# Optimization experiments

Hardware: AMD Instinct MI355X
Metric: run time of the kernel (lower is better)

The kernel has to match this reference:

```python
import jax, jax.numpy as jnp
import numpy as np

B, T, D, W, H = 64, 512, 768, 255, 8
DH = D // H

def layernorm(x, g, b, eps=1e-5):
    m = jnp.mean(x, axis=-1, keepdims=True)
    v = jnp.mean((x - m) ** 2, axis=-1, keepdims=True)
    return (x - m) * jax.lax.rsqrt(v + eps) * g + b

def setup_inputs() -> dict:
    key = jax.random.key(0)
    ks = list(jax.random.split(key, 12))
    p = lambda k, shape, s=0.02: (jax.random.normal(k, shape, jnp.float32) * s)
    # words_ids: -100 at CLS/SEP, each word spans 2 subtokens -> 255 words/row
    wi = np.full((B, T), -100, dtype=np.int32)
    pos = np.arange(1, T - 1)
    wi[:, 1:T - 1] = (pos - 1) // 2
    return {
        'output_bert': jax.random.normal(ks[0], (B, T, D), jnp.float32),
        'words_ids': jnp.asarray(wi),
        'Wq': p(ks[1], (D, D)), 'bq': jnp.zeros((D,), jnp.float32),
        'Wk': p(ks[2], (D, D)), 'bk': jnp.zeros((D,), jnp.float32),
        'Wv': p(ks[3], (D, D)), 'bv': jnp.zeros((D,), jnp.float32),
        'Wo': p(ks[4], (D, D)), 'bo': jnp.zeros((D,), jnp.float32),
        'ln1_g': jnp.ones((D,), jnp.float32), 'ln1_b': jnp.zeros((D,), jnp.float32),
        'W1f': p(ks[5], (D, 4 * D)), 'b1f': jnp.zeros((4 * D,), jnp.float32),
        'W2f': p(ks[6], (4 * D, D)), 'b2f': jnp.zeros((D,), jnp.float32),
        'ln2_g': jnp.ones((D,), jnp.float32), 'ln2_b': jnp.zeros((D,), jnp.float32),
        'ng': jnp.ones((D,), jnp.float32), 'nb': jnp.zeros((D,), jnp.float32),
        'lin_w': p(ks[7], (D, 2)), 'lin_b': jnp.zeros((2,), jnp.float32),
    }

def reference(output_bert, words_ids, Wq, bq, Wk, bk, Wv, bv, Wo, bo,
              ln1_g, ln1_b, W1f, b1f, W2f, b2f, ln2_g, ln2_b, ng, nb, lin_w, lin_b):
    Bsz = output_bert.shape[0]
    # --- first-subtoken gather: first token position of each word id ---
    hits = words_ids[:, None, :] == jnp.arange(W)[None, :, None]   # [B, W, T]
    first_idx = jnp.argmax(hits, axis=-1)                           # [B, W]
    feat = jnp.take_along_axis(output_bert, first_idx[..., None], axis=1)  # [B, W, D]
    # --- transformer encoder layer (post-norm, relu FFN) ---
    q = (feat @ Wq + bq).reshape(Bsz, W, H, DH)
    k = (feat @ Wk + bk).reshape(Bsz, W, H, DH)
    v = (feat @ Wv + bv).reshape(Bsz, W, H, DH)
    scores = jnp.einsum('bqhd,bkhd->bhqk', q, k) * (1.0 / np.sqrt(DH))
    attn = jax.nn.softmax(scores, axis=-1)
    ctx = jnp.einsum('bhqk,bkhd->bqhd', attn, v).reshape(Bsz, W, D)
    x = layernorm(feat + ctx @ Wo + bo, ln1_g, ln1_b)
    ff = jax.nn.relu(x @ W1f + b1f) @ W2f + b2f
    x = layernorm(x + ff, ln2_g, ln2_b)
    # --- final LayerNorm + Linear + softmax + argmax path ---
    x = layernorm(x, ng, nb)
    logits = x @ lin_w + lin_b
    ner_prob = jax.nn.softmax(logits, axis=-1)
    path = jnp.argmax(ner_prob, axis=-1)
    return ner_prob, path
```

## Files before the change

### kernel.cpp

```cpp
#include <hip/hip_runtime.h>
#include <cmath>

#define Bsz 64
#define Tt  512
#define Dd  768
#define Wn  255
#define Hh  8
#define DHd 96
#define NROWS (Bsz*Wn)

typedef _Float16 half_t;
typedef _Float16 f16x8 __attribute__((ext_vector_type(8)));
typedef _Float16 f16x4 __attribute__((ext_vector_type(4)));
typedef float f32x4 __attribute__((ext_vector_type(4)));

#define OFF_QKV 0
#define OFF_WO  5308416
#define OFF_W1  7077888
#define OFF_W2  14155776
#define W2_CSTR 3538944
#define SLOTH 25165824
__device__ __align__(16) half_t g_w16[21233664];

__device__ __forceinline__ void gload16(const half_t* g, half_t* l) {
    __builtin_amdgcn_global_load_lds((const __attribute__((address_space(1))) void*)g,
                                     (__attribute__((address_space(3))) void*)l, 16, 0, 0);
}

template<int N> __device__ __forceinline__ void waitv() {
    if constexpr (N == 0) asm volatile("s_waitcnt vmcnt(0)" ::: "memory");
    else if constexpr (N == 1) asm volatile("s_waitcnt vmcnt(1)" ::: "memory");
    else if constexpr (N == 2) asm volatile("s_waitcnt vmcnt(2)" ::: "memory");
    else if constexpr (N == 4) asm volatile("s_waitcnt vmcnt(4)" ::: "memory");
}


__global__ void k_init_fi(int* fi) {
    int i = blockIdx.x * 256 + threadIdx.x;
    if (i < Bsz * Wn) fi[i] = 0x7fffffff;
}

__global__ void k_scan(const int* __restrict__ wid, int* __restrict__ fi) {
    int i = blockIdx.x * 256 + threadIdx.x;
    if (i >= Bsz * Tt) return;
    int b = i / Tt, t = i % Tt;
    int w = wid[i];
    if (w >= 0 && w < Wn) atomicMin(&fi[b * Wn + w], t);
}

__global__ void k_bcat(const float* __restrict__ bq, const float* __restrict__ bk,
                       const float* __restrict__ bv, float* __restrict__ o) {
    int i = blockIdx.x * 256 + threadIdx.x;
    if (i < 768) o[i] = bq[i];
    else if (i < 1536) o[i] = bk[i - 768];
    else if (i < 2304) o[i] = bv[i - 1536];
}

__global__ void k_gather(const float4* __restrict__ ob, const int* __restrict__ fi,
                         half_t* __restrict__ f16) {
    int i = blockIdx.x * 256 + threadIdx.x;
    if (i >= NROWS * 192) return;
    int r = i / 192, c = i % 192;
    int b = r / Wn;
    int idx = fi[r];
    if (idx == 0x7fffffff) idx = 0;
    float4 v = ob[((size_t)b * Tt + idx) * 192 + c];
    float a0 = v.x * 16.f, a1 = v.y * 16.f, a2 = v.z * 16.f, a3 = v.w * 16.f;
    half_t h0 = (half_t)a0, h1 = (half_t)a1, h2 = (half_t)a2, h3 = (half_t)a3;
    f16x4 hv = {h0, h1, h2, h3};
    f16x4 lv = {(half_t)(a0 - (float)h0), (half_t)(a1 - (float)h1),
                (half_t)(a2 - (float)h2), (half_t)(a3 - (float)h3)};
    size_t off = (size_t)r * 1536 + c * 4;
    *(f16x4*)&f16[off] = hv;
    *(f16x4*)&f16[off + 768] = lv;
}


__global__ void k_wsplit(const float* __restrict__ Wm, int K, int N,
                         size_t obase, int Kseg, size_t cstride) {
    __shared__ float sm[32][33];
    const int tx = threadIdx.x, ty = threadIdx.y;
    const int n0 = blockIdx.x * 32, k0 = blockIdx.y * 32;
    #pragma unroll
    for (int r = 0; r < 4; ++r)
        sm[ty + r * 8][tx] = Wm[(size_t)(k0 + ty + r * 8) * N + n0 + tx];
    __syncthreads();
    #pragma unroll
    for (int r = 0; r < 4; ++r) {
        float v = 64.f * sm[tx][ty + r * 8];
        half_t hi = (half_t)v;
        half_t lo = (half_t)(v - (float)hi);
        int k = k0 + tx;
        int n = n0 + ty + r * 8;
        int c = k / Kseg, kk = k - c * Kseg;
        half_t* o = g_w16 + obase + (size_t)c * cstride + (size_t)n * (3 * Kseg) + kk;
        o[0] = hi; o[Kseg] = hi; o[2 * Kseg] = lo;
    }
}


__device__ __forceinline__ void stage_b(const half_t* B, int Kp3, int col0,
                                        int t, int c, half_t* dst, int tid) {
    int gc = col0 + c * 64 + (tid >> 3);
    int sj = (tid & 7) ^ ((tid >> 3) & 7);
    gload16(B + (size_t)gc * Kp3 + (size_t)t * 64 + sj * 8,
            dst + 8192 + c * 4096 + (tid >> 6) * 512);
}

__device__ __forceinline__ void stage_a0(const half_t* Ap, int lda, int row0, int M,
                                         int kk, int c, half_t* dst, int tid) {
    int gr = row0 + c * 64 + (tid >> 3); if (gr > M - 1) gr = M - 1;
    int sj = (tid & 7) ^ ((tid >> 3) & 7);
    gload16(Ap + (size_t)gr * lda + kk + sj * 8, dst + c * 4096 + (tid >> 6) * 512);
}

__device__ __forceinline__ void stage_a1(const half_t* qcb, int row0, int M,
                                         int kk, int soff, int c, half_t* dst, int tid) {
    int gr = row0 + c * 64 + (tid >> 3); if (gr > M - 1) gr = M - 1;
    int sj = (tid & 7) ^ ((tid >> 3) & 7);
    int k = kk + sj * 8;
    int h = k / 96, d = k - h * 96;
    int b = gr / 255, wl = gr - b * 255;
    gload16(qcb + ((size_t)(b * 8 + h) * 256 + wl) * 192 + d + soff,
            dst + c * 4096 + (tid >> 6) * 512);
}

template<int MODE, int AMODE>
__global__ __launch_bounds__(512, 4) void k_gemm128(
    const half_t* __restrict__ Ah, const half_t* __restrict__ Al, int lda,
    size_t boff, const float* __restrict__ bias,
    const void* res, void* out0, void* out1,
    int M, int N, int K) {
    __shared__ half_t sm[2][20480];
    const int tid = threadIdx.x;
    const int w = tid >> 6, l = tid & 63;
    const int wm = w >> 2, wn = w & 3;
    const int fr = l & 15, q4 = l >> 4;
    const int ck0 = (q4 * 8) ^ ((fr & 7) << 3);
    const int ck1 = ck0 ^ 32;
    const half_t* Bsrc = g_w16 + boff;
    const int Kp3 = 3 * K, NT = Kp3 >> 6;

    int lin = blockIdx.y * gridDim.x + blockIdx.x;
    int nwg = gridDim.x * gridDim.y;
    int wg = (lin & 7) * (nwg >> 3) + (lin >> 3);
    int by = wg / gridDim.x, bx = wg - by * gridDim.x;
    const int row0 = by * 128, col0 = bx * 192;

    f32x4 acc[4][3];
    #pragma unroll
    for (int m = 0; m < 4; ++m)
        #pragma unroll
        for (int j = 0; j < 3; ++j) acc[m][j] = (f32x4){0.f, 0.f, 0.f, 0.f};

    {
        half_t* d0 = &sm[0][0];
        stage_b(Bsrc, Kp3, col0, 0, 0, d0, tid);
        stage_b(Bsrc, Kp3, col0, 0, 1, d0, tid);
        if (AMODE == 0) {
            stage_a0(Ah, lda, row0, M, 0, 0, d0, tid);
            stage_a0(Ah, lda, row0, M, 0, 1, d0, tid);
        } else {
            stage_a1(Ah, row0, M, 0, 0, 0, d0, tid);
            stage_a1(Ah, row0, M, 0, 0, 1, d0, tid);
        }
        stage_b(Bsrc, Kp3, col0, 0, 2, d0, tid);
    }
    waitv<1>();
    __builtin_amdgcn_s_barrier();
    asm volatile("" ::: "memory");

    for (int t = 0; t < NT; ++t) {
        const int p = t & 1;
        half_t* nxt = &sm[p ^ 1][0];
        const half_t* pA = &sm[p][wm * 4096];
        const half_t* pB = &sm[p][8192];
        const int tn = t + 1;
        const bool pf = tn < NT;
        const int segn = (tn * 64 >= 2 * K) ? 2 : ((tn * 64 >= K) ? 1 : 0);
        const int kkn = tn * 64 - segn * K;
        const half_t* An = (segn == 1) ? Al : Ah;
        const int soff = (segn == 1) ? 96 : 0;

        f16x8 b0[2], b1[2], a0[4], a1[4];
        #pragma unroll
        for (int j = 0; j < 2; ++j) {
            const half_t* p_ = &pB[j * 4096 + (wn * 16 + fr) * 64];
            b0[j] = *(const f16x8*)&p_[ck0];
            b1[j] = *(const f16x8*)&p_[ck1];
        }
        #pragma unroll
        for (int m = 0; m < 4; ++m) {
            a0[m] = *(const f16x8*)&pA[m * 1024 + fr * 64 + ck0];
            a1[m] = *(const f16x8*)&pA[m * 1024 + fr * 64 + ck1];
        }
        if (pf) {
            stage_b(Bsrc, Kp3, col0, tn, 0, nxt, tid);
            stage_b(Bsrc, Kp3, col0, tn, 1, nxt, tid);
            if (AMODE == 0) {
                stage_a0(An, lda, row0, M, kkn, 0, nxt, tid);
                stage_a0(An, lda, row0, M, kkn, 1, nxt, tid);
            } else {
                stage_a1(Ah, row0, M, kkn, soff, 0, nxt, tid);
                stage_a1(Ah, row0, M, kkn, soff, 1, nxt, tid);
            }
        }
        __builtin_amdgcn_s_setprio(1);
        #pragma unroll
        for (int m = 0; m < 4; ++m)
            #pragma unroll
            for (int j = 0; j < 2; ++j) {
                acc[m][j] = __builtin_amdgcn_mfma_f32_16x16x32_f16(a0[m], b0[j], acc[m][j], 0, 0, 0);
                acc[m][j] = __builtin_amdgcn_mfma_f32_16x16x32_f16(a1[m], b1[j], acc[m][j], 0, 0, 0);
            }
        __builtin_amdgcn_s_setprio(0);
        if (pf) waitv<4>();
        else    waitv<0>();
        __builtin_amdgcn_s_barrier();
        asm volatile("" ::: "memory");

        f16x8 c0, c1;
        {
            const half_t* p_ = &pB[2 * 4096 + (wn * 16 + fr) * 64];
            c0 = *(const f16x8*)&p_[ck0];
            c1 = *(const f16x8*)&p_[ck1];
        }
        if (pf) stage_b(Bsrc, Kp3, col0, tn, 2, nxt, tid);
        __builtin_amdgcn_s_setprio(1);
        #pragma unroll
        for (int m = 0; m < 4; ++m) {
            acc[m][2] = __builtin_amdgcn_mfma_f32_16x16x32_f16(a0[m], c0, acc[m][2], 0, 0, 0);
            acc[m][2] = __builtin_amdgcn_mfma_f32_16x16x32_f16(a1[m], c1, acc[m][2], 0, 0, 0);
        }
        __builtin_amdgcn_s_setprio(0);
        if (pf) {
            waitv<1>();
            __builtin_amdgcn_s_barrier();
            asm volatile("" ::: "memory");
        }
    }

    const float dsc = 1.0f / 1024.0f;
    #pragma unroll
    for (int m = 0; m < 4; ++m) {
        #pragma unroll
        for (int r = 0; r < 4; ++r) {
            const int row = row0 + wm * 64 + m * 16 + q4 * 4 + r;
            if (row >= M) continue;
            #pragma unroll
            for (int j = 0; j < 3; ++j) {
                const int col = col0 + j * 64 + wn * 16 + fr;
                float vv = acc[m][j][r] * dsc;
                if (MODE != 4) vv += bias[col];
                if (MODE == 5) {
                    int part = col / 768, cc = col - part * 768;
                    int h = cc / 96, d = cc - h * 96;
                    int b = row / 255, wl = row - b * 255;
                    float t16 = vv * 16.f;
                    half_t hi = (half_t)t16;
                    half_t lo = (half_t)(t16 - (float)hi);
                    half_t* dstp = (half_t*)out0 + (size_t)part * SLOTH;
                    size_t o = ((size_t)(b * 8 + h) * 256 + wl) * 192 + d;
                    dstp[o] = hi; dstp[o + 96] = lo;
                } else if (MODE == 1) {
                    const half_t* rp = (const half_t*)res;
                    vv += ((float)rp[(size_t)row * 1536 + col] +
                           (float)rp[(size_t)row * 1536 + 768 + col]) * 0.0625f;
                    ((float*)out0)[(size_t)row * N + col] = vv;
                } else if (MODE == 2) {
                    vv = fmaxf(vv, 0.f);
                    float t16 = vv * 16.f;
                    half_t hi = (half_t)t16;
                    ((half_t*)out0)[(size_t)row * N + col] = hi;
                    ((half_t*)out1)[(size_t)row * N + col] = (half_t)(t16 - (float)hi);
                } else if (MODE == 3) {
                    vv += ((const float*)res)[(size_t)row * N + col];
                    ((float*)out0)[(size_t)row * N + col] = vv;
                } else {
                    float* op = (float*)out0 + (size_t)row * N + col;
                    *op += vv;
                }
            }
        }
    }
}


__global__ __launch_bounds__(256, 2) void k_attn2(half_t* __restrict__ qc,
                                                  const half_t* __restrict__ kk16,
                                                  const half_t* __restrict__ vv16) {
    __shared__ half_t sK[64][200];
    __shared__ half_t sVT[192][72];
    __shared__ float  sP[4][16][68];
    const int tid = threadIdx.x;
    const int w = tid >> 6, l = tid & 63;
    const int lr = l & 15, lc = l >> 4;
    const size_t base = (size_t)blockIdx.x * 49152;
    const float ssc = 0.10206207261596575f / 256.0f;

    for (int pass = 0; pass < 2; ++pass) {
        f32x4 O[2][6];
        float mrow[2][4], lrow[2][4];
        #pragma unroll
        for (int qs = 0; qs < 2; ++qs) {
            #pragma unroll
            for (int dn = 0; dn < 6; ++dn) O[qs][dn] = (f32x4){0.f, 0.f, 0.f, 0.f};
            #pragma unroll
            for (int r = 0; r < 4; ++r) { mrow[qs][r] = -3e38f; lrow[qs][r] = 0.f; }
        }
        for (int kt = 0; kt < 4; ++kt) {
            __syncthreads();
            #pragma unroll
            for (int c = 0; c < 6; ++c) {
                int ch = w + c * 4;
                *(f16x8*)&sK[l][ch * 8] =
                    *(const f16x8*)(kk16 + base + (size_t)(kt * 64 + l) * 192 + ch * 8);
            }
            #pragma unroll
            for (int c = 0; c < 6; ++c) {
                int ch = w + c * 4;
                f16x8 vv = *(const f16x8*)(vv16 + base + (size_t)(kt * 64 + l) * 192 + ch * 8);
                #pragma unroll
                for (int j = 0; j < 8; ++j) sVT[ch * 8 + j][l] = vv[j];
            }
            __syncthreads();
            #pragma unroll
            for (int qs = 0; qs < 2; ++qs) {
                const int qrow0 = (pass * 2 + qs) * 64 + w * 16;
                f16x8 qf0[3], qf1[3];
                #pragma unroll
                for (int s = 0; s < 3; ++s) {
                    qf0[s] = *(const f16x8*)(qc + base + (size_t)(qrow0 + lr) * 192 + s * 32 + lc * 8);
                    qf1[s] = *(const f16x8*)(qc + base + (size_t)(qrow0 + lr) * 192 + 96 + s * 32 + lc * 8);
                }
                f32x4 sacc[4];
                #pragma unroll
                for (int nt = 0; nt < 4; ++nt) sacc[nt] = (f32x4){0.f, 0.f, 0.f, 0.f};
                #pragma unroll
                for (int s = 0; s < 3; ++s)
                    #pragma unroll
                    for (int nt = 0; nt < 4; ++nt) {
                        f16x8 kh = *(const f16x8*)&sK[nt * 16 + lr][s * 32 + lc * 8];
                        f16x8 klo = *(const f16x8*)&sK[nt * 16 + lr][96 + s * 32 + lc * 8];
                        sacc[nt] = __builtin_amdgcn_mfma_f32_16x16x32_f16(qf0[s], kh, sacc[nt], 0, 0, 0);
                        sacc[nt] = __builtin_amdgcn_mfma_f32_16x16x32_f16(qf0[s], klo, sacc[nt], 0, 0, 0);
                        sacc[nt] = __builtin_amdgcn_mfma_f32_16x16x32_f16(qf1[s], kh, sacc[nt], 0, 0, 0);
                    }
                float sv[4][4], mx[4] = {-3e38f, -3e38f, -3e38f, -3e38f};
                #pragma unroll
                for (int nt = 0; nt < 4; ++nt) {
                    int key = kt * 64 + nt * 16 + lr;
                    #pragma unroll
                    for (int r = 0; r < 4; ++r) {
                        float s_ = sacc[nt][r] * ssc;
                        if (key >= 255) s_ = -3e38f;
                        sv[nt][r] = s_;
                        mx[r] = fmaxf(mx[r], s_);
                    }
                }
                #pragma unroll
                for (int r = 0; r < 4; ++r) {
                    mx[r] = fmaxf(mx[r], __shfl_xor(mx[r], 1));
                    mx[r] = fmaxf(mx[r], __shfl_xor(mx[r], 2));
                    mx[r] = fmaxf(mx[r], __shfl_xor(mx[r], 4));
                    mx[r] = fmaxf(mx[r], __shfl_xor(mx[r], 8));
                }
                float alpha[4], rsum[4];
                #pragma unroll
                for (int r = 0; r < 4; ++r) {
                    float mn = fmaxf(mrow[qs][r], mx[r]);
                    alpha[r] = __expf(mrow[qs][r] - mn);
                    mrow[qs][r] = mn;
                    rsum[r] = 0.f;
                }
                float pv[4][4];
                #pragma unroll
                for (int nt = 0; nt < 4; ++nt)
                    #pragma unroll
                    for (int r = 0; r < 4; ++r) {
                        float p = __expf(sv[nt][r] - mrow[qs][r]);
                        pv[nt][r] = p;
                        rsum[r] += p;
                    }
                #pragma unroll
                for (int r = 0; r < 4; ++r) {
                    rsum[r] += __shfl_xor(rsum[r], 1);
                    rsum[r] += __shfl_xor(rsum[r], 2);
                    rsum[r] += __shfl_xor(rsum[r], 4);
                    rsum[r] += __shfl_xor(rsum[r], 8);
                    lrow[qs][r] = lrow[qs][r] * alpha[r] + rsum[r];
                }
                #pragma unroll
                for (int dn = 0; dn < 6; ++dn)
                    #pragma unroll
                    for (int r = 0; r < 4; ++r) O[qs][dn][r] *= alpha[r];
                #pragma unroll
                for (int nt = 0; nt < 4; ++nt)
                    #pragma unroll
                    for (int r = 0; r < 4; ++r)
                        sP[w][lc * 4 + r][nt * 16 + lr] = pv[nt][r];
                #pragma unroll
                for (int ks = 0; ks < 2; ++ks) {
                    const float* pp = &sP[w][lr][ks * 32 + lc * 8];
                    f16x8 ph, pl;
                    #pragma unroll
                    for (int j = 0; j < 8; ++j) {
                        float p = pp[j];
                        half_t h_ = (half_t)p;
                        ph[j] = h_;
                        pl[j] = (half_t)(p - (float)h_);
                    }
                    #pragma unroll
                    for (int dn = 0; dn < 6; ++dn) {
                        f16x8 vh = *(const f16x8*)&sVT[dn * 16 + lr][ks * 32 + lc * 8];
                        f16x8 vl = *(const f16x8*)&sVT[96 + dn * 16 + lr][ks * 32 + lc * 8];
                        O[qs][dn] = __builtin_amdgcn_mfma_f32_16x16x32_f16(ph, vh, O[qs][dn], 0, 0, 0);
                        O[qs][dn] = __builtin_amdgcn_mfma_f32_16x16x32_f16(ph, vl, O[qs][dn], 0, 0, 0);
                        O[qs][dn] = __builtin_amdgcn_mfma_f32_16x16x32_f16(pl, vh, O[qs][dn], 0, 0, 0);
                    }
                }
            }
        }
        #pragma unroll
        for (int qs = 0; qs < 2; ++qs) {
            const int qrow0 = (pass * 2 + qs) * 64 + w * 16;
            #pragma unroll
            for (int r = 0; r < 4; ++r) {
                int qrow = qrow0 + lc * 4 + r;
                if (qrow >= Wn) continue;
                float inv = 1.0f / lrow[qs][r];
                #pragma unroll
                for (int dn = 0; dn < 6; ++dn) {
                    float val = O[qs][dn][r] * inv;
                    half_t hi = (half_t)val;
                    half_t lo = (half_t)(val - (float)hi);
                    size_t o = base + (size_t)qrow * 192 + dn * 16 + lr;
                    qc[o] = hi;
                    qc[o + 96] = lo;
                }
            }
        }
    }
}


__global__ __launch_bounds__(256) void k_ln1(const float* __restrict__ X, const float* __restrict__ g,
                                             const float* __restrict__ bt, float* __restrict__ Y,
                                             half_t* __restrict__ Y16) {
    const int r = blockIdx.x, tid = threadIdx.x;
    __shared__ float red[256];
    const float* x = X + (size_t)r * Dd;
    float x0 = x[tid], x1 = x[tid + 256], x2 = x[tid + 512];
    red[tid] = x0 + x1 + x2; __syncthreads();
    for (int s = 128; s > 0; s >>= 1) { if (tid < s) red[tid] += red[tid + s]; __syncthreads(); }
    float mean = red[0] * (1.0f / 768.0f);
    __syncthreads();
    float d0 = x0 - mean, d1 = x1 - mean, d2 = x2 - mean;
    red[tid] = d0 * d0 + d1 * d1 + d2 * d2; __syncthreads();
    for (int s = 128; s > 0; s >>= 1) { if (tid < s) red[tid] += red[tid + s]; __syncthreads(); }
    float rs = rsqrtf(red[0] * (1.0f / 768.0f) + 1e-5f);
    float* y = Y + (size_t)r * Dd;
    float y0 = d0 * rs * g[tid]       + bt[tid];
    float y1 = d1 * rs * g[tid + 256] + bt[tid + 256];
    float y2 = d2 * rs * g[tid + 512] + bt[tid + 512];
    y[tid] = y0; y[tid + 256] = y1; y[tid + 512] = y2;
    half_t* h = Y16 + (size_t)r * 1536;
    float t0 = y0 * 16.f, t1 = y1 * 16.f, t2 = y2 * 16.f;
    half_t h0 = (half_t)t0, h1 = (half_t)t1, h2 = (half_t)t2;
    h[tid] = h0; h[tid + 256] = h1; h[tid + 512] = h2;
    h[768 + tid] = (half_t)(t0 - (float)h0);
    h[768 + tid + 256] = (half_t)(t1 - (float)h1);
    h[768 + tid + 512] = (half_t)(t2 - (float)h2);
}


__global__ __launch_bounds__(256) void k_lnfinal(const float* __restrict__ X,
                                                 const float* __restrict__ g2, const float* __restrict__ b2,
                                                 const float* __restrict__ ng, const float* __restrict__ nb,
                                                 const float* __restrict__ lw, const float* __restrict__ lb,
                                                 float* __restrict__ out) {
    const int r = blockIdx.x, tid = threadIdx.x;
    __shared__ float red[256];
    const float* x = X + (size_t)r * Dd;
    float x0 = x[tid], x1 = x[tid + 256], x2 = x[tid + 512];
    red[tid] = x0 + x1 + x2; __syncthreads();
    for (int s = 128; s > 0; s >>= 1) { if (tid < s) red[tid] += red[tid + s]; __syncthreads(); }
    float mean = red[0] * (1.0f / 768.0f);
    __syncthreads();
    float d0 = x0 - mean, d1 = x1 - mean, d2 = x2 - mean;
    red[tid] = d0 * d0 + d1 * d1 + d2 * d2; __syncthreads();
    for (int s = 128; s > 0; s >>= 1) { if (tid < s) red[tid] += red[tid + s]; __syncthreads(); }
    float rs = rsqrtf(red[0] * (1.0f / 768.0f) + 1e-5f);
    __syncthreads();
    float y0 = d0 * rs * g2[tid]       + b2[tid];
    float y1 = d1 * rs * g2[tid + 256] + b2[tid + 256];
    float y2 = d2 * rs * g2[tid + 512] + b2[tid + 512];
    red[tid] = y0 + y1 + y2; __syncthreads();
    for (int s = 128; s > 0; s >>= 1) { if (tid < s) red[tid] += red[tid + s]; __syncthreads(); }
    float mean2 = red[0] * (1.0f / 768.0f);
    __syncthreads();
    float e0 = y0 - mean2, e1 = y1 - mean2, e2 = y2 - mean2;
    red[tid] = e0 * e0 + e1 * e1 + e2 * e2; __syncthreads();
    for (int s = 128; s > 0; s >>= 1) { if (tid < s) red[tid] += red[tid + s]; __syncthreads(); }
    float rs2 = rsqrtf(red[0] * (1.0f / 768.0f) + 1e-5f);
    __syncthreads();
    float n0 = e0 * rs2 * ng[tid]       + nb[tid];
    float n1 = e1 * rs2 * ng[tid + 256] + nb[tid + 256];
    float n2 = e2 * rs2 * ng[tid + 512] + nb[tid + 512];
    float l0 = n0 * lw[2 * tid]     + n1 * lw[2 * (tid + 256)]     + n2 * lw[2 * (tid + 512)];
    float l1 = n0 * lw[2 * tid + 1] + n1 * lw[2 * (tid + 256) + 1] + n2 * lw[2 * (tid + 512) + 1];
    red[tid] = l0; __syncthreads();
    for (int s = 128; s > 0; s >>= 1) { if (tid < s) red[tid] += red[tid + s]; __syncthreads(); }
    l0 = red[0]; __syncthreads();
    red[tid] = l1; __syncthreads();
    for (int s = 128; s > 0; s >>= 1) { if (tid < s) red[tid] += red[tid + s]; __syncthreads(); }
    l1 = red[0];
    if (tid == 0) {
        l0 += lb[0]; l1 += lb[1];
        float m = fmaxf(l0, l1);
        float e0_ = expf(l0 - m), e1_ = expf(l1 - m);
        float inv = 1.0f / (e0_ + e1_);
        out[2 * r] = e0_ * inv;
        out[2 * r + 1] = e1_ * inv;
        out[2 * NROWS + r] = (l1 > l0) ? 1.0f : 0.0f;
    }
}


extern "C" void kernel_launch(void* const* d_in, const int* in_sizes, int n_in,
                              void* d_out, int out_size, void* d_ws, size_t ws_size,
                              hipStream_t stream) {
    const float* ob  = (const float*)d_in[0];
    const int*   wid = (const int*)d_in[1];
    const float* Wq  = (const float*)d_in[2];  const float* bq  = (const float*)d_in[3];
    const float* Wk  = (const float*)d_in[4];  const float* bk  = (const float*)d_in[5];
    const float* Wv  = (const float*)d_in[6];  const float* bv  = (const float*)d_in[7];
    const float* Wo  = (const float*)d_in[8];  const float* bo  = (const float*)d_in[9];
    const float* g1  = (const float*)d_in[10]; const float* b1  = (const float*)d_in[11];
    const float* W1f = (const float*)d_in[12]; const float* b1f = (const float*)d_in[13];
    const float* W2f = (const float*)d_in[14]; const float* b2f = (const float*)d_in[15];
    const float* g2  = (const float*)d_in[16]; const float* b2  = (const float*)d_in[17];
    const float* ng  = (const float*)d_in[18]; const float* nb  = (const float*)d_in[19];
    const float* lw  = (const float*)d_in[20]; const float* lb  = (const float*)d_in[21];
    float* out = (float*)d_out;

    char* ws = (char*)d_ws;
    const size_t MB = 1u << 20;
    const size_t SLOT = 48 * MB;
    int* fi = (int*)ws;
    float* bcat = (float*)(ws + 262144);
    char* S1 = ws + MB;
    char* S2 = S1 + SLOT;
    char* S3 = S2 + SLOT;
    char* S4 = S3 + SLOT;

    half_t* feat16 = (half_t*)S1;
    half_t* q16    = (half_t*)S2;
    half_t* k16    = (half_t*)S3;
    half_t* v16    = (half_t*)S4;
    float*  t1     = (float*)S3;
    float*  xbuf   = (float*)S4;
    half_t* x16    = (half_t*)S2;
    half_t* ffh_h  = (half_t*)S1;
    half_t* ffh_l  = (half_t*)S3;

    k_wsplit<<<dim3(24, 24), dim3(32, 8), 0, stream>>>(Wq, 768, 768, OFF_QKV,                   768, 0);
    k_wsplit<<<dim3(24, 24), dim3(32, 8), 0, stream>>>(Wk, 768, 768, OFF_QKV + 768ul * 2304,    768, 0);
    k_wsplit<<<dim3(24, 24), dim3(32, 8), 0, stream>>>(Wv, 768, 768, OFF_QKV + 1536ul * 2304,   768, 0);
    k_wsplit<<<dim3(24, 24), dim3(32, 8), 0, stream>>>(Wo, 768, 768, OFF_WO,                    768, 0);
    k_wsplit<<<dim3(96, 24), dim3(32, 8), 0, stream>>>(W1f, 768, 3072, OFF_W1,                  768, 0);
    k_wsplit<<<dim3(24, 96), dim3(32, 8), 0, stream>>>(W2f, 3072, 768, OFF_W2,                 1536, W2_CSTR);
    k_bcat<<<9, 256, 0, stream>>>(bq, bk, bv, bcat);

    k_init_fi<<<(Bsz * Wn + 255) / 256, 256, 0, stream>>>(fi);
    k_scan<<<(Bsz * Tt) / 256, 256, 0, stream>>>(wid, fi);
    k_gather<<<(NROWS * 192 + 255) / 256, 256, 0, stream>>>((const float4*)ob, fi, feat16);

    k_gemm128<5, 0><<<dim3(12, 128), 512, 0, stream>>>(
        feat16, feat16 + 768, 1536, OFF_QKV, bcat, nullptr, q16, nullptr, NROWS, 2304, 768);

    k_attn2<<<Bsz * Hh, 256, 0, stream>>>(q16, k16, v16);

    k_gemm128<1, 1><<<dim3(4, 128), 512, 0, stream>>>(
        q16, q16 + 96, 0, OFF_WO, bo, feat16, t1, nullptr, NROWS, 768, 768);
    k_ln1<<<NROWS, 256, 0, stream>>>(t1, g1, b1, xbuf, x16);

    for (int c = 0; c < 2; ++c) {
        k_gemm128<2, 0><<<dim3(8, 128), 512, 0, stream>>>(
            x16, x16 + 768, 1536, OFF_W1 + (size_t)c * 1536 * 2304, b1f + c * 1536,
            nullptr, ffh_h, ffh_l, NROWS, 1536, 768);
        if (c == 0)
            k_gemm128<3, 0><<<dim3(4, 128), 512, 0, stream>>>(
                ffh_h, ffh_l, 1536, OFF_W2, b2f, xbuf, xbuf, nullptr, NROWS, 768, 1536);
        else
            k_gemm128<4, 0><<<dim3(4, 128), 512, 0, stream>>>(
                ffh_h, ffh_l, 1536, OFF_W2 + (size_t)W2_CSTR, b2f,
                nullptr, xbuf, nullptr, NROWS, 768, 1536);
    }

    k_lnfinal<<<NROWS, 256, 0, stream>>>(xbuf, g2, b2, ng, nb, lw, lb, out);
}
```

Measured before the change: 1.191 ms.

## Enlarge GEMM tile to 256x192 with four-phase pipelined k-loop

Replaces the 128x192 GEMM kernel with a 256x192 variant. Each wave now holds 8x3 accumulators, and the k-step is split into four phases that interleave LDS reads of A subtiles, staging of the next tile, barriers and MFMA bursts. The larger tile raises reuse of each B tile loaded and halves the grid. In exchange it uses more registers and LDS, lowers occupancy to 2 blocks per CU, and the M=16320 grid (64 row blocks) may leave CUs unevenly loaded.

```diff
diff --git a/kernel.cpp b/kernel.cpp
--- a/kernel.cpp
+++ b/kernel.cpp
@@ -29,7 +29,6 @@
 
 template<int N> __device__ __forceinline__ void waitv() {
     if constexpr (N == 0) asm volatile("s_waitcnt vmcnt(0)" ::: "memory");
-    else if constexpr (N == 1) asm volatile("s_waitcnt vmcnt(1)" ::: "memory");
     else if constexpr (N == 2) asm volatile("s_waitcnt vmcnt(2)" ::: "memory");
     else if constexpr (N == 4) asm volatile("s_waitcnt vmcnt(4)" ::: "memory");
 }
@@ -104,7 +103,7 @@
     int gc = col0 + c * 64 + (tid >> 3);
     int sj = (tid & 7) ^ ((tid >> 3) & 7);
     gload16(B + (size_t)gc * Kp3 + (size_t)t * 64 + sj * 8,
-            dst + 8192 + c * 4096 + (tid >> 6) * 512);
+            dst + 16384 + c * 4096 + (tid >> 6) * 512);
 }
 
 __device__ __forceinline__ void stage_a0(const half_t* Ap, int lda, int row0, int M,
@@ -125,13 +124,37 @@
             dst + c * 4096 + (tid >> 6) * 512);
 }
 
+#define PH_READA(Q) do { \
+    _Pragma("unroll") \
+    for (int mt = 0; mt < 2; ++mt) { \
+        const half_t* p_ = &pA[aBase + ((Q) / 2) * 4096 + (((Q) % 2) * 32 + mt * 16 + fr) * 64]; \
+        a0[mt] = *(const f16x8*)&p_[ck0]; \
+        a1[mt] = *(const f16x8*)&p_[ck1]; \
+    } } while (0)
+
+#define PH_MFMA(Q) do { \
+    __builtin_amdgcn_s_setprio(1); \
+    _Pragma("unroll") \
+    for (int mt = 0; mt < 2; ++mt) { \
+        _Pragma("unroll") \
+        for (int j = 0; j < 3; ++j) { \
+            acc[2 * (Q) + mt][j] = __builtin_amdgcn_mfma_f32_16x16x32_f16(a0[mt], b0[j], acc[2 * (Q) + mt][j], 0, 0, 0); \
+            acc[2 * (Q) + mt][j] = __builtin_amdgcn_mfma_f32_16x16x32_f16(a1[mt], b1[j], acc[2 * (Q) + mt][j], 0, 0, 0); \
+        } } \
+    __builtin_amdgcn_s_setprio(0); } while (0)
+
+#define PH_SYNC() do { \
+    __builtin_amdgcn_s_barrier(); \
+    asm volatile("s_waitcnt lgkmcnt(0)" ::: "memory"); \
+    __builtin_amdgcn_sched_barrier(0); } while (0)
+
 template<int MODE, int AMODE>
-__global__ __launch_bounds__(512, 4) void k_gemm128(
+__global__ __launch_bounds__(512, 2) void k_gemm256p(
     const half_t* __restrict__ Ah, const half_t* __restrict__ Al, int lda,
     size_t boff, const float* __restrict__ bias,
     const void* res, void* out0, void* out1,
     int M, int N, int K) {
-    __shared__ half_t sm[2][20480];
+    __shared__ half_t sm[2][28672];
     const int tid = threadIdx.x;
     const int w = tid >> 6, l = tid & 63;
     const int wm = w >> 2, wn = w & 3;
@@ -140,16 +163,17 @@
     const int ck1 = ck0 ^ 32;
     const half_t* Bsrc = g_w16 + boff;
     const int Kp3 = 3 * K, NT = Kp3 >> 6;
+    const int aBase = wm * 8192;
 
     int lin = blockIdx.y * gridDim.x + blockIdx.x;
     int nwg = gridDim.x * gridDim.y;
     int wg = (lin & 7) * (nwg >> 3) + (lin >> 3);
     int by = wg / gridDim.x, bx = wg - by * gridDim.x;
-    const int row0 = by * 128, col0 = bx * 192;
-
-    f32x4 acc[4][3];
+    const int row0 = by * 256, col0 = bx * 192;
+
+    f32x4 acc[8][3];
     #pragma unroll
-    for (int m = 0; m < 4; ++m)
+    for (int m = 0; m < 8; ++m)
         #pragma unroll
         for (int j = 0; j < 3; ++j) acc[m][j] = (f32x4){0.f, 0.f, 0.f, 0.f};
 
@@ -157,24 +181,28 @@
         half_t* d0 = &sm[0][0];
         stage_b(Bsrc, Kp3, col0, 0, 0, d0, tid);
         stage_b(Bsrc, Kp3, col0, 0, 1, d0, tid);
+        stage_b(Bsrc, Kp3, col0, 0, 2, d0, tid);
         if (AMODE == 0) {
             stage_a0(Ah, lda, row0, M, 0, 0, d0, tid);
+            stage_a0(Ah, lda, row0, M, 0, 2, d0, tid);
             stage_a0(Ah, lda, row0, M, 0, 1, d0, tid);
+            stage_a0(Ah, lda, row0, M, 0, 3, d0, tid);
         } else {
             stage_a1(Ah, row0, M, 0, 0, 0, d0, tid);
+            stage_a1(Ah, row0, M, 0, 0, 2, d0, tid);
             stage_a1(Ah, row0, M, 0, 0, 1, d0, tid);
-        }
-        stage_b(Bsrc, Kp3, col0, 0, 2, d0, tid);
+            stage_a1(Ah, row0, M, 0, 0, 3, d0, tid);
+        }
     }
-    waitv<1>();
+    waitv<2>();
     __builtin_amdgcn_s_barrier();
     asm volatile("" ::: "memory");
 
     for (int t = 0; t < NT; ++t) {
         const int p = t & 1;
         half_t* nxt = &sm[p ^ 1][0];
-        const half_t* pA = &sm[p][wm * 4096];
-        const half_t* pB = &sm[p][8192];
+        const half_t* pA = &sm[p][0];
+        const half_t* pB = &sm[p][16384];
         const int tn = t + 1;
         const bool pf = tn < NT;
         const int segn = (tn * 64 >= 2 * K) ? 2 : ((tn * 64 >= K) ? 1 : 0);
@@ -182,70 +210,68 @@
         const half_t* An = (segn == 1) ? Al : Ah;
         const int soff = (segn == 1) ? 96 : 0;
 
-        f16x8 b0[2], b1[2], a0[4], a1[4];
+        f16x8 b0[3], b1[3], a0[2], a1[2];
+
         #pragma unroll
-        for (int j = 0; j < 2; ++j) {
+        for (int j = 0; j < 3; ++j) {
             const half_t* p_ = &pB[j * 4096 + (wn * 16 + fr) * 64];
             b0[j] = *(const f16x8*)&p_[ck0];
             b1[j] = *(const f16x8*)&p_[ck1];
         }
-        #pragma unroll
-        for (int m = 0; m < 4; ++m) {
-            a0[m] = *(const f16x8*)&pA[m * 1024 + fr * 64 + ck0];
-            a1[m] = *(const f16x8*)&pA[m * 1024 + fr * 64 + ck1];
-        }
+        PH_READA(0);
         if (pf) {
             stage_b(Bsrc, Kp3, col0, tn, 0, nxt, tid);
             stage_b(Bsrc, Kp3, col0, tn, 1, nxt, tid);
-            if (AMODE == 0) {
-                stage_a0(An, lda, row0, M, kkn, 0, nxt, tid);
-                stage_a0(An, lda, row0, M, kkn, 1, nxt, tid);
-            } else {
-                stage_a1(Ah, row0, M, kkn, soff, 0, nxt, tid);
-                stage_a1(Ah, row0, M, kkn, soff, 1, nxt, tid);
-            }
-        }
-        __builtin_amdgcn_s_setprio(1);
-        #pragma unroll
-        for (int m = 0; m < 4; ++m)
-            #pragma unroll
-            for (int j = 0; j < 2; ++j) {
-                acc[m][j] = __builtin_amdgcn_mfma_f32_16x16x32_f16(a0[m], b0[j], acc[m][j], 0, 0, 0);
-                acc[m][j] = __builtin_amdgcn_mfma_f32_16x16x32_f16(a1[m], b1[j], acc[m][j], 0, 0, 0);
-            }
-        __builtin_amdgcn_s_setprio(0);
+        }
+        PH_SYNC();
+        PH_MFMA(0);
+        __builtin_amdgcn_s_barrier();
+
+        PH_READA(1);
+        if (pf) {
+            stage_b(Bsrc, Kp3, col0, tn, 2, nxt, tid);
+            if (AMODE == 0) stage_a0(An, lda, row0, M, kkn, 0, nxt, tid);
+            else            stage_a1(Ah, row0, M, kkn, soff, 0, nxt, tid);
+        }
+        PH_SYNC();
+        PH_MFMA(1);
         if (pf) waitv<4>();
         else    waitv<0>();
         __builtin_amdgcn_s_barrier();
-        asm volatile("" ::: "memory");
-
-        f16x8 c0, c1;
-        {
-            const half_t* p_ = &pB[2 * 4096 + (wn * 16 + fr) * 64];
-            c0 = *(const f16x8*)&p_[ck0];
-            c1 = *(const f16x8*)&p_[ck1];
-        }
-        if (pf) stage_b(Bsrc, Kp3, col0, tn, 2, nxt, tid);
-        __builtin_amdgcn_s_setprio(1);
-        #pragma unroll
-        for (int m = 0; m < 4; ++m) {
-            acc[m][2] = __builtin_amdgcn_mfma_f32_16x16x32_f16(a0[m], c0, acc[m][2], 0, 0, 0);
-            acc[m][2] = __builtin_amdgcn_mfma_f32_16x16x32_f16(a1[m], c1, acc[m][2], 0, 0, 0);
-        }
-        __builtin_amdgcn_s_setprio(0);
+
+        PH_READA(2);
         if (pf) {
-            waitv<1>();
+            if (AMODE == 0) {
+                stage_a0(An, lda, row0, M, kkn, 2, nxt, tid);
+                stage_a0(An, lda, row0, M, kkn, 1, nxt, tid);
+            } else {
+                stage_a1(Ah, row0, M, kkn, soff, 2, nxt, tid);
+                stage_a1(Ah, row0, M, kkn, soff, 1, nxt, tid);
+            }
+        }
+        PH_SYNC();
+        PH_MFMA(2);
+        __builtin_amdgcn_s_barrier();
+
+        PH_READA(3);
+        if (pf) {
+            if (AMODE == 0) stage_a0(An, lda, row0, M, kkn, 3, nxt, tid);
+            else            stage_a1(Ah, row0, M, kkn, soff, 3, nxt, tid);
+        }
+        PH_SYNC();
+        PH_MFMA(3);
+        if (pf) {
+            waitv<2>();
             __builtin_amdgcn_s_barrier();
-            asm volatile("" ::: "memory");
         }
     }
 
     const float dsc = 1.0f / 1024.0f;
     #pragma unroll
-    for (int m = 0; m < 4; ++m) {
+    for (int m = 0; m < 8; ++m) {
         #pragma unroll
         for (int r = 0; r < 4; ++r) {
-            const int row = row0 + wm * 64 + m * 16 + q4 * 4 + r;
+            const int row = row0 + wm * 128 + m * 16 + q4 * 4 + r;
             if (row >= M) continue;
             #pragma unroll
             for (int j = 0; j < 3; ++j) {
@@ -576,24 +602,24 @@
     k_scan<<<(Bsz * Tt) / 256, 256, 0, stream>>>(wid, fi);
     k_gather<<<(NROWS * 192 + 255) / 256, 256, 0, stream>>>((const float4*)ob, fi, feat16);
 
-    k_gemm128<5, 0><<<dim3(12, 128), 512, 0, stream>>>(
+    k_gemm256p<5, 0><<<dim3(12, 64), 512, 0, stream>>>(
         feat16, feat16 + 768, 1536, OFF_QKV, bcat, nullptr, q16, nullptr, NROWS, 2304, 768);
 
     k_attn2<<<Bsz * Hh, 256, 0, stream>>>(q16, k16, v16);
 
-    k_gemm128<1, 1><<<dim3(4, 128), 512, 0, stream>>>(
+    k_gemm256p<1, 1><<<dim3(4, 64), 512, 0, stream>>>(
         q16, q16 + 96, 0, OFF_WO, bo, feat16, t1, nullptr, NROWS, 768, 768);
     k_ln1<<<NROWS, 256, 0, stream>>>(t1, g1, b1, xbuf, x16);
 
     for (int c = 0; c < 2; ++c) {
-        k_gemm128<2, 0><<<dim3(8, 128), 512, 0, stream>>>(
+        k_gemm256p<2, 0><<<dim3(8, 64), 512, 0, stream>>>(
             x16, x16 + 768, 1536, OFF_W1 + (size_t)c * 1536 * 2304, b1f + c * 1536,
             nullptr, ffh_h, ffh_l, NROWS, 1536, 768);
         if (c == 0)
-            k_gemm128<3, 0><<<dim3(4, 128), 512, 0, stream>>>(
+            k_gemm256p<3, 0><<<dim3(4, 64), 512, 0, stream>>>(
                 ffh_h, ffh_l, 1536, OFF_W2, b2f, xbuf, xbuf, nullptr, NROWS, 768, 1536);
         else
-            k_gemm128<4, 0><<<dim3(4, 128), 512, 0, stream>>>(
+            k_gemm256p<4, 0><<<dim3(4, 64), 512, 0, stream>>>(
                 ffh_h, ffh_l, 1536, OFF_W2 + (size_t)W2_CSTR, b2f,
                 nullptr, xbuf, nullptr, NROWS, 768, 1536);
     }
```

New measurement: 1.200 ms. About the same (+0.7%).
